# Kernel tuning notes

Measured on AMD Instinct MI355X. Metric: run time of the kernel, lower is better.

## Reference

```python
import jax, jax.numpy as jnp
import numpy as np

HIDDEN = 1024
N_HEADS = 16
HEAD_DIM = HIDDEN // N_HEADS


def setup_inputs() -> dict:
    key = jax.random.key(0)
    ks = jax.random.split(key, 10)
    s = 0.02
    return {
        "x": jax.random.normal(ks[0], (2, 2048, HIDDEN), dtype=jnp.float32),
        "wq_w": jax.random.normal(ks[1], (HEAD_DIM, HEAD_DIM), dtype=jnp.float32) * s,
        "wq_b": jax.random.normal(ks[2], (HEAD_DIM,), dtype=jnp.float32) * s,
        "wk_w": jax.random.normal(ks[3], (HEAD_DIM, HEAD_DIM), dtype=jnp.float32) * s,
        "wk_b": jax.random.normal(ks[4], (HEAD_DIM,), dtype=jnp.float32) * s,
        "wv_w": jax.random.normal(ks[5], (HEAD_DIM, HEAD_DIM), dtype=jnp.float32) * s,
        "wv_b": jax.random.normal(ks[6], (HEAD_DIM,), dtype=jnp.float32) * s,
        "wo_w": jax.random.normal(ks[7], (HIDDEN, HIDDEN), dtype=jnp.float32) * s,
        "wo_b": jax.random.normal(ks[8], (HIDDEN,), dtype=jnp.float32) * s,
    }


def reference(x, wq_w, wq_b, wk_w, wk_b, wv_w, wv_b, wo_w, wo_b):
    B, S, _ = x.shape
    # Faithful to torch: plain reshape (view), NOT a transpose-based head split.
    xh = x.reshape(B, N_HEADS, S, HEAD_DIM)  # [B,H,S,D]
    # torch Linear: y = x @ W.T + b
    Q = jnp.einsum('bhsd,ed->bhse', xh, wq_w) + wq_b
    K = jnp.einsum('bhsd,ed->bhse', xh, wk_w) + wk_b
    V = jnp.einsum('bhsd,ed->bhse', xh, wv_w) + wv_b
    scale = 1.0 / jnp.sqrt(jnp.float32(HEAD_DIM))
    scores = jnp.einsum('bhqd,bhkd->bhqk', Q, K) * scale  # [B,H,S,S]
    attn = jax.nn.softmax(scores, axis=-1)
    ctx = jnp.einsum('bhqk,bhkd->bhqd', attn, V)  # [B,H,S,D]
    out = ctx.reshape(B, S, HIDDEN)
    return out @ wo_w.T + wo_b
```

## Files before the change

### kernel.cpp

```cpp
#include <hip/hip_runtime.h>
#include <hip/hip_bf16.h>

#define SEQ 2048
#define BHCOUNT 32
#define NROWS (BHCOUNT*SEQ)

typedef unsigned short u16;
typedef unsigned int u32;
using bf16x8 = __attribute__((ext_vector_type(8))) short;
using f32x4  = __attribute__((ext_vector_type(4))) float;

__device__ __forceinline__ float bf2f(u16 h) {
    return __uint_as_float(((u32)h) << 16);
}
__device__ __forceinline__ u16 f2bf(float f) {
    u32 u = __float_as_uint(f);
    u32 r = (u + 0x7FFFu + ((u >> 16) & 1u)) >> 16;
    return (u16)r;
}
__device__ __forceinline__ float fexp2(float x) {
    float r; asm("v_exp_f32 %0, %1" : "=v"(r) : "v"(x)); return r;
}

__device__ __forceinline__ void gload16(const u16* g, u16* l) {
    __builtin_amdgcn_global_load_lds(
        (const __attribute__((address_space(1))) u32*)g,
        (__attribute__((address_space(3))) u32*)l, 16, 0, 0);
}

__device__ __forceinline__ void cvt8(const float* src, float sc, u16* o) {
    float4 a = *(const float4*)src;
    float4 b = *(const float4*)(src + 4);
    o[0]=f2bf(a.x*sc); o[1]=f2bf(a.y*sc); o[2]=f2bf(a.z*sc); o[3]=f2bf(a.w*sc);
    o[4]=f2bf(b.x*sc); o[5]=f2bf(b.y*sc); o[6]=f2bf(b.z*sc); o[7]=f2bf(b.w*sc);
}

__global__ __launch_bounds__(256) void qkv_wconv_kernel(
    const float* __restrict__ x,
    const float* __restrict__ wq, const float* __restrict__ bq,
    const float* __restrict__ wk, const float* __restrict__ bk,
    const float* __restrict__ wv, const float* __restrict__ bv,
    const float* __restrict__ wo,
    u16* __restrict__ Q, u16* __restrict__ K, u16* __restrict__ Vg,
    u16* __restrict__ wob_t)
{
    __shared__ u16 xs[128*64];
    __shared__ u16 ws[192*64];
    __shared__ float bs[192];
    const int t = threadIdx.x;

    if (blockIdx.x >= 512) {
        int g = (blockIdx.x - 512)*256 + t;
        int tile = g >> 9, within = g & 511;
        int row = within >> 3, ks = within & 7;
        int cb = tile >> 4, kt = tile & 15;
        u16 o[8];
        cvt8(&wo[(size_t)(cb*64 + row)*1024 + kt*64 + ks*8], 1.f, o);
        *(uint4*)&wob_t[(size_t)g*8] = *(uint4*)o;
        return;
    }

    const int wid = t >> 6, lane = t & 63;
    const int ln = lane & 15, g4 = lane >> 4;
    const int blk = blockIdx.x;
    const int m0 = blk * 128;
    const int bh = blk >> 4;
    const int ktg0 = (blk & 15) * 2;
    const float qscale = 0.125f * 1.44269504f;

    #pragma unroll
    for (int c = 0; c < 6; ++c) {
        int slot = c*256 + t;
        int row = slot >> 3, ks = slot & 7;
        const float* wsrc = (c < 2) ? wq : (c < 4) ? wk : wv;
        float sc = (c < 2) ? qscale : 1.f;
        u16 o[8];
        cvt8(&wsrc[(row & 63)*64 + ks*8], sc, o);
        *(uint4*)&ws[row*64 + ((ks ^ (row & 7)) << 3)] = *(uint4*)o;
    }
    #pragma unroll
    for (int c = 0; c < 4; ++c) {
        int slot = c*256 + t;
        int row = slot >> 3, ks = slot & 7;
        u16 o[8];
        cvt8(&x[(size_t)(m0 + row)*64 + ks*8], 1.f, o);
        *(uint4*)&xs[row*64 + ((ks ^ (row & 7)) << 3)] = *(uint4*)o;
    }
    if (t < 192) {
        int p = t >> 6, e = t & 63;
        bs[t] = (p == 0) ? bq[e]*qscale : (p == 1) ? bk[e] : bv[e];
    }
    __syncthreads();

    bf16x8 af[2][2];
    #pragma unroll
    for (int mf = 0; mf < 2; ++mf)
        #pragma unroll
        for (int kf = 0; kf < 2; ++kf) {
            int arow = wid*32 + mf*16 + ln;
            af[mf][kf] = *(const bf16x8*)&xs[arow*64 + (((kf*4 + g4) ^ (arow & 7)) << 3)];
        }

    #pragma unroll
    for (int p = 0; p < 2; ++p) {
        bf16x8 bfr[4][2];
        #pragma unroll
        for (int nt = 0; nt < 4; ++nt)
            #pragma unroll
            for (int kf = 0; kf < 2; ++kf) {
                int brow = p*64 + nt*16 + ln;
                bfr[nt][kf] = *(const bf16x8*)&ws[brow*64 + (((kf*4 + g4) ^ (ln & 7)) << 3)];
            }
        f32x4 acc[2][4];
        #pragma unroll
        for (int mf = 0; mf < 2; ++mf)
            #pragma unroll
            for (int nt = 0; nt < 4; ++nt) acc[mf][nt] = (f32x4){0.f,0.f,0.f,0.f};
        #pragma unroll
        for (int kf = 0; kf < 2; ++kf)
            #pragma unroll
            for (int mf = 0; mf < 2; ++mf)
                #pragma unroll
                for (int nt = 0; nt < 4; ++nt)
                    acc[mf][nt] = __builtin_amdgcn_mfma_f32_16x16x32_bf16(
                        af[mf][kf], bfr[nt][kf], acc[mf][nt], 0, 0, 0);
        u16* dst = p ? K : Q;
        #pragma unroll
        for (int mf = 0; mf < 2; ++mf)
            #pragma unroll
            for (int nt = 0; nt < 4; ++nt) {
                float bv4 = bs[p*64 + nt*16 + ln];
                #pragma unroll
                for (int r = 0; r < 4; ++r)
                    dst[(size_t)(m0 + wid*32 + mf*16 + g4*4 + r)*64 + nt*16 + ln]
                        = f2bf(acc[mf][nt][r] + bv4);
            }
    }

    bf16x8 wvf[4][2];
    #pragma unroll
    for (int et = 0; et < 4; ++et)
        #pragma unroll
        for (int kf = 0; kf < 2; ++kf) {
            int brow = 128 + et*16 + ln;
            wvf[et][kf] = *(const bf16x8*)&ws[brow*64 + (((kf*4 + g4) ^ (ln & 7)) << 3)];
        }
    f32x4 vacc[4][2];
    #pragma unroll
    for (int et = 0; et < 4; ++et)
        #pragma unroll
        for (int st = 0; st < 2; ++st) vacc[et][st] = (f32x4){0.f,0.f,0.f,0.f};
    #pragma unroll
    for (int kf = 0; kf < 2; ++kf)
        #pragma unroll
        for (int et = 0; et < 4; ++et)
            #pragma unroll
            for (int st = 0; st < 2; ++st)
                vacc[et][st] = __builtin_amdgcn_mfma_f32_16x16x32_bf16(
                    wvf[et][kf], af[st][kf], vacc[et][st], 0, 0, 0);

    __syncthreads();
    u16* vstage = xs;
    #pragma unroll
    for (int et = 0; et < 4; ++et)
        #pragma unroll
        for (int st = 0; st < 2; ++st)
            #pragma unroll
            for (int r = 0; r < 4; ++r) {
                int e = et*16 + g4*4 + r;
                int s = wid*32 + st*16 + ln;
                vstage[e*128 + ((s + 2*e) & 127)] = f2bf(vacc[et][st][r] + bs[128 + e]);
            }
    __syncthreads();

    #pragma unroll
    for (int c = 0; c < 8; ++c) {
        int j = c*256 + t;
        int kt2 = j >> 10, within = j & 1023;
        int ee = within >> 4, kp0 = (within & 15) * 4;
        int sbase = ((kp0 & 4) << 3) | ((kp0 & 32) >> 1) | ((kp0 & 24) >> 1);
        u16 o[4];
        #pragma unroll
        for (int i = 0; i < 4; ++i)
            o[i] = vstage[ee*128 + ((kt2*64 + sbase + i + 2*ee) & 127)];
        *(uint2*)&Vg[((size_t)bh*32 + ktg0 + kt2)*4096 + ee*64 + kp0] = *(uint2*)o;
    }
}

__global__ __launch_bounds__(256, 4) void attn_kernel(
    const u16* __restrict__ Q, const u16* __restrict__ K,
    const u16* __restrict__ Vg, u16* __restrict__ ctx)
{
    __shared__ u16 Kls[2][4096];
    __shared__ u16 Vls[2][4096];

    const int t = threadIdx.x;
    const int wid = t >> 6, lane = t & 63;
    const int ln = lane & 15, g4 = lane >> 4;
    const int bh = blockIdx.y;
    const size_t base   = (size_t)bh * SEQ * 64;
    const size_t vgbase = (size_t)bh * 32 * 4096;
    const int q0 = blockIdx.x * 64 + wid * 16;

    int goff[2];
    #pragma unroll
    for (int c = 0; c < 2; ++c) {
        int s = c*256 + t;
        int row = s >> 3, ks = s & 7;
        goff[c] = row*64 + ((ks ^ (row & 7)) << 3);
    }

    int foff[4][2];
    #pragma unroll
    for (int nt = 0; nt < 4; ++nt)
        #pragma unroll
        for (int kf = 0; kf < 2; ++kf) {
            int frow = nt*16 + ln;
            foff[nt][kf] = frow*64 + (((kf*4 + g4) ^ (frow & 7)) << 3);
        }

    bf16x8 qf[2];
    #pragma unroll
    for (int kf = 0; kf < 2; ++kf)
        qf[kf] = *(const bf16x8*)&Q[base + (size_t)(q0 + ln)*64 + kf*32 + g4*8];

    bf16x8 ones;
    #pragma unroll
    for (int i = 0; i < 8; ++i) ones[i] = (short)0x3F80;

    f32x4 oacc[4];
    #pragma unroll
    for (int i = 0; i < 4; ++i) oacc[i] = (f32x4){0.f, 0.f, 0.f, 0.f};
    f32x4 lacc = (f32x4){0.f, 0.f, 0.f, 0.f};

    #pragma unroll
    for (int c = 0; c < 2; ++c) {
        gload16(&K [base   + goff[c]], &Kls[0][c*2048 + wid*512]);
        gload16(&Vg[vgbase + goff[c]], &Vls[0][c*2048 + wid*512]);
    }
    __syncthreads();

    for (int kt2 = 0; kt2 < 16; ++kt2) {
        #pragma unroll
        for (int half = 0; half < 2; ++half) {
            const int kt = kt2*2 + half;
            if (kt < 31) {
                #pragma unroll
                for (int c = 0; c < 2; ++c) {
                    gload16(&K [base   + (size_t)(kt+1)*4096 + goff[c]],
                            &Kls[half^1][c*2048 + wid*512]);
                    gload16(&Vg[vgbase + (size_t)(kt+1)*4096 + goff[c]],
                            &Vls[half^1][c*2048 + wid*512]);
                }
            }
            const u16* Ks  = Kls[half];
            const u16* Vts = Vls[half];

            f32x4 sacc[4];
            #pragma unroll
            for (int nt = 0; nt < 4; ++nt) sacc[nt] = (f32x4){0.f, 0.f, 0.f, 0.f};
            __builtin_amdgcn_s_setprio(1);
            #pragma unroll
            for (int nt = 0; nt < 4; ++nt)
                #pragma unroll
                for (int kf = 0; kf < 2; ++kf)
                    sacc[nt] = __builtin_amdgcn_mfma_f32_16x16x32_bf16(
                        *(const bf16x8*)&Ks[foff[nt][kf]], qf[kf], sacc[nt], 0, 0, 0);
            __builtin_amdgcn_s_setprio(0);

            #pragma unroll
            for (int nt = 0; nt < 4; ++nt)
                #pragma unroll
                for (int r = 0; r < 4; ++r)
                    sacc[nt][r] = fexp2(sacc[nt][r]);

            union PU { u32 w[4]; bf16x8 v; } pu0, pu1;
            asm("v_cvt_pk_bf16_f32 %0, %1, %2" : "=v"(pu0.w[0]) : "v"(sacc[0][0]), "v"(sacc[0][1]));
            asm("v_cvt_pk_bf16_f32 %0, %1, %2" : "=v"(pu0.w[1]) : "v"(sacc[0][2]), "v"(sacc[0][3]));
            asm("v_cvt_pk_bf16_f32 %0, %1, %2" : "=v"(pu0.w[2]) : "v"(sacc[2][0]), "v"(sacc[2][1]));
            asm("v_cvt_pk_bf16_f32 %0, %1, %2" : "=v"(pu0.w[3]) : "v"(sacc[2][2]), "v"(sacc[2][3]));
            asm("v_cvt_pk_bf16_f32 %0, %1, %2" : "=v"(pu1.w[0]) : "v"(sacc[1][0]), "v"(sacc[1][1]));
            asm("v_cvt_pk_bf16_f32 %0, %1, %2" : "=v"(pu1.w[1]) : "v"(sacc[1][2]), "v"(sacc[1][3]));
            asm("v_cvt_pk_bf16_f32 %0, %1, %2" : "=v"(pu1.w[2]) : "v"(sacc[3][0]), "v"(sacc[3][1]));
            asm("v_cvt_pk_bf16_f32 %0, %1, %2" : "=v"(pu1.w[3]) : "v"(sacc[3][2]), "v"(sacc[3][3]));
            bf16x8 pf[2] = { pu0.v, pu1.v };

            __builtin_amdgcn_s_setprio(1);
            #pragma unroll
            for (int dt = 0; dt < 4; ++dt)
                #pragma unroll
                for (int kf = 0; kf < 2; ++kf)
                    oacc[dt] = __builtin_amdgcn_mfma_f32_16x16x32_bf16(
                        pf[kf], *(const bf16x8*)&Vts[foff[dt][kf]], oacc[dt], 0, 0, 0);
            #pragma unroll
            for (int kf = 0; kf < 2; ++kf)
                lacc = __builtin_amdgcn_mfma_f32_16x16x32_bf16(pf[kf], ones, lacc, 0, 0, 0);
            __builtin_amdgcn_s_setprio(0);

            __syncthreads();
        }
    }

    #pragma unroll
    for (int r = 0; r < 4; ++r) {
        float inv = 1.f / lacc[r];
        size_t row = base + (size_t)(q0 + g4*4 + r)*64;
        #pragma unroll
        for (int dt = 0; dt < 4; ++dt)
            ctx[row + dt*16 + ln] = f2bf(oacc[dt][r] * inv);
    }
}

__global__ __launch_bounds__(256) void oproj_kernel(
    const u16* __restrict__ ctx, const u16* __restrict__ wob_t,
    const float* __restrict__ bo, float* __restrict__ out)
{
    __shared__ u16 Als[2][128*64];
    __shared__ u16 Bls[2][64*64];
    const int t = threadIdx.x;
    const int wid = t >> 6, lane = t & 63;
    const int ln = lane & 15, g4 = lane >> 4;
    const int wr = wid >> 1, wc = wid & 1;
    const int rb = blockIdx.x, cb = blockIdx.y;
    const int m0 = rb * 128;

    int gA[4], gB[2];
    #pragma unroll
    for (int c = 0; c < 4; ++c) {
        int slot = c*256 + t;
        int row = slot >> 3, ks = slot & 7;
        gA[c] = row*1024 + ((ks ^ (row & 7)) << 3);
    }
    #pragma unroll
    for (int c = 0; c < 2; ++c) {
        int slot = c*256 + t;
        int row = slot >> 3, ks = slot & 7;
        gB[c] = row*64 + ((ks ^ (row & 7)) << 3);
    }
    const u16* actx = ctx + (size_t)m0*1024;
    const u16* bw   = wob_t + (size_t)cb*16*4096;

    f32x4 acc[4][2];
    #pragma unroll
    for (int mf = 0; mf < 4; ++mf)
        #pragma unroll
        for (int nf = 0; nf < 2; ++nf)
            acc[mf][nf] = (f32x4){0.f, 0.f, 0.f, 0.f};

    #pragma unroll
    for (int c = 0; c < 4; ++c) gload16(&actx[gA[c]], &Als[0][(c*256+t)*8]);
    #pragma unroll
    for (int c = 0; c < 2; ++c) gload16(&bw[gB[c]],   &Bls[0][(c*256+t)*8]);
    __syncthreads();

    for (int kt2 = 0; kt2 < 8; ++kt2) {
        #pragma unroll
        for (int half = 0; half < 2; ++half) {
            const int kt = kt2*2 + half;
            if (kt < 15) {
                #pragma unroll
                for (int c = 0; c < 4; ++c)
                    gload16(&actx[(kt+1)*64 + gA[c]], &Als[half^1][(c*256+t)*8]);
                #pragma unroll
                for (int c = 0; c < 2; ++c)
                    gload16(&bw[(kt+1)*4096 + gB[c]], &Bls[half^1][(c*256+t)*8]);
            }
            const u16* As = Als[half];
            const u16* Bs = Bls[half];

            __builtin_amdgcn_s_setprio(1);
            #pragma unroll
            for (int kf = 0; kf < 2; ++kf) {
                bf16x8 af[4], bfr[2];
                #pragma unroll
                for (int mf = 0; mf < 4; ++mf) {
                    int arow = wr*64 + mf*16 + ln;
                    af[mf] = *(const bf16x8*)&As[arow*64 + (((kf*4 + g4) ^ (arow & 7)) << 3)];
                }
                #pragma unroll
                for (int nf = 0; nf < 2; ++nf) {
                    int brow = wc*32 + nf*16 + ln;
                    bfr[nf] = *(const bf16x8*)&Bs[brow*64 + (((kf*4 + g4) ^ (brow & 7)) << 3)];
                }
                #pragma unroll
                for (int mf = 0; mf < 4; ++mf)
                    #pragma unroll
                    for (int nf = 0; nf < 2; ++nf)
                        acc[mf][nf] = __builtin_amdgcn_mfma_f32_16x16x32_bf16(
                            af[mf], bfr[nf], acc[mf][nf], 0, 0, 0);
            }
            __builtin_amdgcn_s_setprio(0);

            __syncthreads();
        }
    }

    #pragma unroll
    for (int mf = 0; mf < 4; ++mf)
        #pragma unroll
        for (int r = 0; r < 4; ++r) {
            int m = m0 + wr*64 + mf*16 + g4*4 + r;
            #pragma unroll
            for (int nf = 0; nf < 2; ++nf) {
                int col = cb*64 + wc*32 + nf*16 + ln;
                out[(size_t)m*1024 + col] = acc[mf][nf][r] + bo[col];
            }
        }
}

extern "C" void kernel_launch(void* const* d_in, const int* in_sizes, int n_in,
                              void* d_out, int out_size, void* d_ws, size_t ws_size,
                              hipStream_t stream) {
    (void)in_sizes; (void)n_in; (void)out_size; (void)ws_size;
    const float* x  = (const float*)d_in[0];
    const float* wq = (const float*)d_in[1];
    const float* bq = (const float*)d_in[2];
    const float* wk = (const float*)d_in[3];
    const float* bk = (const float*)d_in[4];
    const float* wv = (const float*)d_in[5];
    const float* bv = (const float*)d_in[6];
    const float* wo = (const float*)d_in[7];
    const float* bo = (const float*)d_in[8];
    float* out = (float*)d_out;

    u16* Qb  = (u16*)d_ws;
    u16* Kb  = Qb + (size_t)NROWS*64;
    u16* Vgb = Kb + (size_t)NROWS*64;
    u16* ctx = Vgb + (size_t)NROWS*64;
    u16* wob_t = ctx + (size_t)NROWS*64;

    qkv_wconv_kernel<<<dim3(1024), 256, 0, stream>>>(
        x, wq, bq, wk, bk, wv, bv, wo, Qb, Kb, Vgb, wob_t);
    attn_kernel<<<dim3(32, 32), 256, 0, stream>>>(Qb, Kb, Vgb, ctx);
    oproj_kernel<<<dim3(32, 16), 256, 0, stream>>>(ctx, wob_t, bo, out);
}
```

Before: 76.54 us.

## Switch attention to 32x32x16 MFMA with two-wave blocks of 32 queries each

Rewrites the attention inner loop to use 32x32x16 bf16 MFMAs instead of 16x16x32, with each wave owning 32 query rows and blocks shrunk to 128 threads. The V staging layout permutation in the projection kernel changes to match the new fragment ordering. Larger MFMA tiles raise operand reuse per LDS read and cut instruction count. In exchange, fewer waves per block each carry larger accumulators, which adds register pressure, and each thread issues more of the async K/V loads.

```diff
diff --git a/kernel.cpp b/kernel.cpp
--- a/kernel.cpp
+++ b/kernel.cpp
@@ -9,6 +9,7 @@
 typedef unsigned int u32;
 using bf16x8 = __attribute__((ext_vector_type(8))) short;
 using f32x4  = __attribute__((ext_vector_type(4))) float;
+using f32x16 = __attribute__((ext_vector_type(16))) float;
 
 __device__ __forceinline__ float bf2f(u16 h) {
     return __uint_as_float(((u32)h) << 16);
@@ -178,7 +179,7 @@
         int j = c*256 + t;
         int kt2 = j >> 10, within = j & 1023;
         int ee = within >> 4, kp0 = (within & 15) * 4;
-        int sbase = ((kp0 & 4) << 3) | ((kp0 & 32) >> 1) | ((kp0 & 24) >> 1);
+        int sbase = (kp0 & 48) + (((kp0 >> 3) & 1) << 2) + (((kp0 >> 2) & 1) << 3);
         u16 o[4];
         #pragma unroll
         for (int i = 0; i < 4; ++i)
@@ -187,7 +188,7 @@
     }
 }
 
-__global__ __launch_bounds__(256, 4) void attn_kernel(
+__global__ __launch_bounds__(128, 2) void attn_kernel(
     const u16* __restrict__ Q, const u16* __restrict__ K,
     const u16* __restrict__ Vg, u16* __restrict__ ctx)
 {
@@ -196,47 +197,46 @@
 
     const int t = threadIdx.x;
     const int wid = t >> 6, lane = t & 63;
-    const int ln = lane & 15, g4 = lane >> 4;
+    const int l31 = lane & 31, h = lane >> 5;
     const int bh = blockIdx.y;
     const size_t base   = (size_t)bh * SEQ * 64;
     const size_t vgbase = (size_t)bh * 32 * 4096;
-    const int q0 = blockIdx.x * 64 + wid * 16;
-
-    int goff[2];
-    #pragma unroll
-    for (int c = 0; c < 2; ++c) {
-        int s = c*256 + t;
+    const int q0 = blockIdx.x * 64 + wid * 32;
+
+    int goff[4];
+    #pragma unroll
+    for (int c = 0; c < 4; ++c) {
+        int s = c*128 + t;
         int row = s >> 3, ks = s & 7;
         goff[c] = row*64 + ((ks ^ (row & 7)) << 3);
     }
 
-    int foff[4][2];
-    #pragma unroll
-    for (int nt = 0; nt < 4; ++nt)
-        #pragma unroll
-        for (int kf = 0; kf < 2; ++kf) {
-            int frow = nt*16 + ln;
-            foff[nt][kf] = frow*64 + (((kf*4 + g4) ^ (frow & 7)) << 3);
-        }
-
-    bf16x8 qf[2];
-    #pragma unroll
-    for (int kf = 0; kf < 2; ++kf)
-        qf[kf] = *(const bf16x8*)&Q[base + (size_t)(q0 + ln)*64 + kf*32 + g4*8];
+    int foff[2][4];
+    #pragma unroll
+    for (int a = 0; a < 2; ++a)
+        #pragma unroll
+        for (int b = 0; b < 4; ++b) {
+            int row = a*32 + l31;
+            foff[a][b] = row*64 + (((b*2 + h) ^ (row & 7)) << 3);
+        }
+
+    bf16x8 qf[4];
+    #pragma unroll
+    for (int kc = 0; kc < 4; ++kc)
+        qf[kc] = *(const bf16x8*)&Q[base + (size_t)(q0 + l31)*64 + kc*16 + h*8];
 
     bf16x8 ones;
     #pragma unroll
     for (int i = 0; i < 8; ++i) ones[i] = (short)0x3F80;
 
-    f32x4 oacc[4];
-    #pragma unroll
-    for (int i = 0; i < 4; ++i) oacc[i] = (f32x4){0.f, 0.f, 0.f, 0.f};
-    f32x4 lacc = (f32x4){0.f, 0.f, 0.f, 0.f};
-
-    #pragma unroll
-    for (int c = 0; c < 2; ++c) {
-        gload16(&K [base   + goff[c]], &Kls[0][c*2048 + wid*512]);
-        gload16(&Vg[vgbase + goff[c]], &Vls[0][c*2048 + wid*512]);
+    f32x16 oacc0, oacc1, lacc;
+    #pragma unroll
+    for (int i = 0; i < 16; ++i) { oacc0[i] = 0.f; oacc1[i] = 0.f; lacc[i] = 0.f; }
+
+    #pragma unroll
+    for (int c = 0; c < 4; ++c) {
+        gload16(&K [base   + goff[c]], &Kls[0][c*1024 + wid*512]);
+        gload16(&Vg[vgbase + goff[c]], &Vls[0][c*1024 + wid*512]);
     }
     __syncthreads();
 
@@ -246,55 +246,62 @@
             const int kt = kt2*2 + half;
             if (kt < 31) {
                 #pragma unroll
-                for (int c = 0; c < 2; ++c) {
+                for (int c = 0; c < 4; ++c) {
                     gload16(&K [base   + (size_t)(kt+1)*4096 + goff[c]],
-                            &Kls[half^1][c*2048 + wid*512]);
+                            &Kls[half^1][c*1024 + wid*512]);
                     gload16(&Vg[vgbase + (size_t)(kt+1)*4096 + goff[c]],
-                            &Vls[half^1][c*2048 + wid*512]);
+                            &Vls[half^1][c*1024 + wid*512]);
                 }
             }
             const u16* Ks  = Kls[half];
             const u16* Vts = Vls[half];
 
-            f32x4 sacc[4];
-            #pragma unroll
-            for (int nt = 0; nt < 4; ++nt) sacc[nt] = (f32x4){0.f, 0.f, 0.f, 0.f};
+            f32x16 s0, s1;
+            #pragma unroll
+            for (int i = 0; i < 16; ++i) { s0[i] = 0.f; s1[i] = 0.f; }
             __builtin_amdgcn_s_setprio(1);
             #pragma unroll
-            for (int nt = 0; nt < 4; ++nt)
-                #pragma unroll
-                for (int kf = 0; kf < 2; ++kf)
-                    sacc[nt] = __builtin_amdgcn_mfma_f32_16x16x32_bf16(
-                        *(const bf16x8*)&Ks[foff[nt][kf]], qf[kf], sacc[nt], 0, 0, 0);
+            for (int kc = 0; kc < 4; ++kc)
+                s0 = __builtin_amdgcn_mfma_f32_32x32x16_bf16(
+                    *(const bf16x8*)&Ks[foff[0][kc]], qf[kc], s0, 0, 0, 0);
+            #pragma unroll
+            for (int kc = 0; kc < 4; ++kc)
+                s1 = __builtin_amdgcn_mfma_f32_32x32x16_bf16(
+                    *(const bf16x8*)&Ks[foff[1][kc]], qf[kc], s1, 0, 0, 0);
             __builtin_amdgcn_s_setprio(0);
 
             #pragma unroll
-            for (int nt = 0; nt < 4; ++nt)
-                #pragma unroll
-                for (int r = 0; r < 4; ++r)
-                    sacc[nt][r] = fexp2(sacc[nt][r]);
-
-            union PU { u32 w[4]; bf16x8 v; } pu0, pu1;
-            asm("v_cvt_pk_bf16_f32 %0, %1, %2" : "=v"(pu0.w[0]) : "v"(sacc[0][0]), "v"(sacc[0][1]));
-            asm("v_cvt_pk_bf16_f32 %0, %1, %2" : "=v"(pu0.w[1]) : "v"(sacc[0][2]), "v"(sacc[0][3]));
-            asm("v_cvt_pk_bf16_f32 %0, %1, %2" : "=v"(pu0.w[2]) : "v"(sacc[2][0]), "v"(sacc[2][1]));
-            asm("v_cvt_pk_bf16_f32 %0, %1, %2" : "=v"(pu0.w[3]) : "v"(sacc[2][2]), "v"(sacc[2][3]));
-            asm("v_cvt_pk_bf16_f32 %0, %1, %2" : "=v"(pu1.w[0]) : "v"(sacc[1][0]), "v"(sacc[1][1]));
-            asm("v_cvt_pk_bf16_f32 %0, %1, %2" : "=v"(pu1.w[1]) : "v"(sacc[1][2]), "v"(sacc[1][3]));
-            asm("v_cvt_pk_bf16_f32 %0, %1, %2" : "=v"(pu1.w[2]) : "v"(sacc[3][0]), "v"(sacc[3][1]));
-            asm("v_cvt_pk_bf16_f32 %0, %1, %2" : "=v"(pu1.w[3]) : "v"(sacc[3][2]), "v"(sacc[3][3]));
-            bf16x8 pf[2] = { pu0.v, pu1.v };
+            for (int i = 0; i < 16; ++i) { s0[i] = fexp2(s0[i]); s1[i] = fexp2(s1[i]); }
+
+            union PU { u32 w[4]; bf16x8 v; } p0, p1, p2, p3;
+            asm("v_cvt_pk_bf16_f32 %0, %1, %2" : "=v"(p0.w[0]) : "v"(s0[0]),  "v"(s0[1]));
+            asm("v_cvt_pk_bf16_f32 %0, %1, %2" : "=v"(p0.w[1]) : "v"(s0[2]),  "v"(s0[3]));
+            asm("v_cvt_pk_bf16_f32 %0, %1, %2" : "=v"(p0.w[2]) : "v"(s0[4]),  "v"(s0[5]));
+            asm("v_cvt_pk_bf16_f32 %0, %1, %2" : "=v"(p0.w[3]) : "v"(s0[6]),  "v"(s0[7]));
+            asm("v_cvt_pk_bf16_f32 %0, %1, %2" : "=v"(p1.w[0]) : "v"(s0[8]),  "v"(s0[9]));
+            asm("v_cvt_pk_bf16_f32 %0, %1, %2" : "=v"(p1.w[1]) : "v"(s0[10]), "v"(s0[11]));
+            asm("v_cvt_pk_bf16_f32 %0, %1, %2" : "=v"(p1.w[2]) : "v"(s0[12]), "v"(s0[13]));
+            asm("v_cvt_pk_bf16_f32 %0, %1, %2" : "=v"(p1.w[3]) : "v"(s0[14]), "v"(s0[15]));
+            asm("v_cvt_pk_bf16_f32 %0, %1, %2" : "=v"(p2.w[0]) : "v"(s1[0]),  "v"(s1[1]));
+            asm("v_cvt_pk_bf16_f32 %0, %1, %2" : "=v"(p2.w[1]) : "v"(s1[2]),  "v"(s1[3]));
+            asm("v_cvt_pk_bf16_f32 %0, %1, %2" : "=v"(p2.w[2]) : "v"(s1[4]),  "v"(s1[5]));
+            asm("v_cvt_pk_bf16_f32 %0, %1, %2" : "=v"(p2.w[3]) : "v"(s1[6]),  "v"(s1[7]));
+            asm("v_cvt_pk_bf16_f32 %0, %1, %2" : "=v"(p3.w[0]) : "v"(s1[8]),  "v"(s1[9]));
+            asm("v_cvt_pk_bf16_f32 %0, %1, %2" : "=v"(p3.w[1]) : "v"(s1[10]), "v"(s1[11]));
+            asm("v_cvt_pk_bf16_f32 %0, %1, %2" : "=v"(p3.w[2]) : "v"(s1[12]), "v"(s1[13]));
+            asm("v_cvt_pk_bf16_f32 %0, %1, %2" : "=v"(p3.w[3]) : "v"(s1[14]), "v"(s1[15]));
+            bf16x8 pf[4] = { p0.v, p1.v, p2.v, p3.v };
 
             __builtin_amdgcn_s_setprio(1);
             #pragma unroll
-            for (int dt = 0; dt < 4; ++dt)
-                #pragma unroll
-                for (int kf = 0; kf < 2; ++kf)
-                    oacc[dt] = __builtin_amdgcn_mfma_f32_16x16x32_bf16(
-                        pf[kf], *(const bf16x8*)&Vts[foff[dt][kf]], oacc[dt], 0, 0, 0);
-            #pragma unroll
-            for (int kf = 0; kf < 2; ++kf)
-                lacc = __builtin_amdgcn_mfma_f32_16x16x32_bf16(pf[kf], ones, lacc, 0, 0, 0);
+            for (int c = 0; c < 4; ++c) {
+                oacc0 = __builtin_amdgcn_mfma_f32_32x32x16_bf16(
+                    pf[c], *(const bf16x8*)&Vts[foff[0][c]], oacc0, 0, 0, 0);
+                oacc1 = __builtin_amdgcn_mfma_f32_32x32x16_bf16(
+                    pf[c], *(const bf16x8*)&Vts[foff[1][c]], oacc1, 0, 0, 0);
+                lacc  = __builtin_amdgcn_mfma_f32_32x32x16_bf16(
+                    pf[c], ones, lacc, 0, 0, 0);
+            }
             __builtin_amdgcn_s_setprio(0);
 
             __syncthreads();
@@ -302,12 +309,12 @@
     }
 
     #pragma unroll
-    for (int r = 0; r < 4; ++r) {
+    for (int r = 0; r < 16; ++r) {
+        int q = (r & 3) + 8*(r >> 2) + 4*h;
         float inv = 1.f / lacc[r];
-        size_t row = base + (size_t)(q0 + g4*4 + r)*64;
-        #pragma unroll
-        for (int dt = 0; dt < 4; ++dt)
-            ctx[row + dt*16 + ln] = f2bf(oacc[dt][r] * inv);
+        size_t row = base + (size_t)(q0 + q)*64;
+        ctx[row + l31]      = f2bf(oacc0[r] * inv);
+        ctx[row + 32 + l31] = f2bf(oacc1[r] * inv);
     }
 }
 
@@ -431,6 +438,6 @@
 
     qkv_wconv_kernel<<<dim3(1024), 256, 0, stream>>>(
         x, wq, bq, wk, bk, wv, bv, wo, Qb, Kb, Vgb, wob_t);
-    attn_kernel<<<dim3(32, 32), 256, 0, stream>>>(Qb, Kb, Vgb, ctx);
+    attn_kernel<<<dim3(32, 32), 128, 0, stream>>>(Qb, Kb, Vgb, ctx);
     oproj_kernel<<<dim3(32, 16), 256, 0, stream>>>(ctx, wob_t, bo, out);
 }
```

After: 80.09 us. +4.6%, slower.
